# Performance work log

Measured on AMD Instinct MI355X. Metric: run time of the kernel, lower is better.

The kernel has to match this reference:

```python
import jax, jax.numpy as jnp
import numpy as np

D_MODEL = 1024
D_FF = 4 * D_MODEL
NUM_EXPERTS = 8
TOP_K = 2
TOKENS = 4096


def setup_inputs() -> dict:
    key = jax.random.key(0)
    ks = jax.random.split(key, 8)
    s = 0.02
    x = jax.random.normal(ks[0], (TOKENS, D_MODEL), dtype=jnp.float32)
    Wg = jax.random.normal(ks[1], (D_MODEL, NUM_EXPERTS), dtype=jnp.float32) * s
    bg = jnp.zeros((NUM_EXPERTS,), dtype=jnp.float32)
    W1 = jax.random.normal(ks[2], (NUM_EXPERTS, D_MODEL, D_FF), dtype=jnp.float32) * s
    b1 = jnp.zeros((NUM_EXPERTS, D_FF), dtype=jnp.float32)
    W2 = jax.random.normal(ks[3], (NUM_EXPERTS, D_FF, D_MODEL), dtype=jnp.float32) * s
    b2 = jnp.zeros((NUM_EXPERTS, D_MODEL), dtype=jnp.float32)
    return {"x": x, "Wg": Wg, "bg": bg, "W1": W1, "b1": b1, "W2": W2, "b2": b2}


def reference(x, Wg, bg, W1, b1, W2, b2):
    # Gating: softmax over experts, select top-k indices per token.
    gate_scores = jax.nn.softmax(x @ Wg + bg, axis=-1)        # [T, E]
    _, top_k_idx = jax.lax.top_k(gate_scores, TOP_K)          # [T, K]
    # Binary combine mask: 1 where expert selected (top_k indices are distinct).
    # NOTE: original sums selected expert outputs WITHOUT gate weighting.
    mask = jnp.sum(jax.nn.one_hot(top_k_idx, NUM_EXPERTS, dtype=x.dtype), axis=1)  # [T, E]
    out = jnp.zeros_like(x)
    for e in range(NUM_EXPERTS):  # small fixed expert count
        h = jax.nn.relu(x @ W1[e] + b1[e])                    # [T, 4D]
        y = h @ W2[e] + b2[e]                                 # [T, D]
        out = out + mask[:, e:e + 1] * y
    return out
```

## Files before the change

kernel.cpp:

```cpp
#include <hip/hip_runtime.h>
#include <hip/hip_bf16.h>

#define T_TOKENS 4096
#define DM 1024
#define DF 4096
#define NE 8
#define MAXROWS 9216

typedef float f32x4 __attribute__((ext_vector_type(4)));
typedef short bf16x8 __attribute__((ext_vector_type(8)));

__device__ __forceinline__ unsigned short f2bf(float f) {
    union { float f; unsigned int u; } v; v.f = f;
    unsigned int r = v.u + 0x7fffu + ((v.u >> 16) & 1u);
    return (unsigned short)(r >> 16);
}

__device__ __forceinline__ void g2l16(const void* g, void* l) {
    __builtin_amdgcn_global_load_lds(
        (const __attribute__((address_space(1))) void*)g,
        (__attribute__((address_space(3))) void*)l, 16, 0, 0);
}

__global__ __launch_bounds__(256) void gate_kernel(
    const float* __restrict__ x, const float* __restrict__ Wg, const float* __restrict__ bg,
    int* __restrict__ counts, int* __restrict__ topk)
{
    int wave = threadIdx.x >> 6;
    int lane = threadIdx.x & 63;
    int t = blockIdx.x * 4 + wave;
    float acc[NE];
#pragma unroll
    for (int e = 0; e < NE; e++) acc[e] = 0.f;
    const float* xr = x + (size_t)t * DM;
#pragma unroll
    for (int i = 0; i < DM / 64; i++) {
        int d = lane + i * 64;
        float xv = xr[d];
        const float4* wg = (const float4*)(Wg + d * NE);
        float4 w0 = wg[0], w1 = wg[1];
        acc[0] += xv * w0.x; acc[1] += xv * w0.y; acc[2] += xv * w0.z; acc[3] += xv * w0.w;
        acc[4] += xv * w1.x; acc[5] += xv * w1.y; acc[6] += xv * w1.z; acc[7] += xv * w1.w;
    }
#pragma unroll
    for (int e = 0; e < NE; e++) {
#pragma unroll
        for (int off = 32; off > 0; off >>= 1)
            acc[e] += __shfl_down(acc[e], off);
    }
    if (lane == 0) {
        float lg[NE];
#pragma unroll
        for (int e = 0; e < NE; e++) lg[e] = acc[e] + bg[e];
        int b1i = 0; float b1v = lg[0];
        for (int e = 1; e < NE; e++) if (lg[e] > b1v) { b1v = lg[e]; b1i = e; }
        int b2i = -1; float b2v = -1e30f;
        for (int e = 0; e < NE; e++) {
            if (e == b1i) continue;
            if (b2i < 0 || lg[e] > b2v) { b2v = lg[e]; b2i = e; }
        }
        topk[t * 2 + 0] = b1i;
        topk[t * 2 + 1] = b2i;
        atomicAdd(&counts[b1i], 1);
        atomicAdd(&counts[b2i], 1);
    }
}

__global__ __launch_bounds__(256) void scatter_kernel(
    const int* __restrict__ counts, const int* __restrict__ topk,
    int* __restrict__ offsets, int* __restrict__ list)
{
    __shared__ int offs[NE + 1];
    __shared__ int cur[NE];
    if (threadIdx.x == 0) {
        int s = 0;
        for (int e = 0; e < NE; e++) {
            offs[e] = s; offsets[e] = s;
            s += (counts[e] + 127) & ~127;
        }
        offs[NE] = s; offsets[NE] = s;
    }
    if (threadIdx.x < NE) cur[threadIdx.x] = 0;
    __syncthreads();
    for (int i = threadIdx.x; i < T_TOKENS * 2; i += 256) {
        int e = topk[i];
        int pos = atomicAdd(&cur[e], 1);
        list[offs[e] + pos] = i >> 1;
    }
    __syncthreads();
    for (int e = 0; e < NE; e++) {
        int s = offs[e] + counts[e];
        int t = offs[e + 1];
        for (int i = s + threadIdx.x; i < t; i += 256) list[i] = -1;
    }
}

__global__ __launch_bounds__(256) void cvt_x_kernel(
    const float* __restrict__ x, unsigned short* __restrict__ xb)
{
    int i = (blockIdx.x * 256 + threadIdx.x) * 4;
    float4 v = *(const float4*)(x + i);
    unsigned short o[4] = { f2bf(v.x), f2bf(v.y), f2bf(v.z), f2bf(v.w) };
    *(uint2*)(xb + i) = *(const uint2*)o;
}

__global__ __launch_bounds__(256) void tr_cvt_kernel(
    const float* __restrict__ src, unsigned short* __restrict__ dst, int K, int N)
{
    const int e = blockIdx.z;
    src += (size_t)e * K * N;
    dst += (size_t)e * N * K;
    const int n0 = blockIdx.x * 64, k0 = blockIdx.y * 64;
    __shared__ unsigned short tile[64][68];
    const int t = threadIdx.x;
    const int tx = t & 63, ty = t >> 6;
#pragma unroll
    for (int r = 0; r < 16; r++) {
        int k = ty * 16 + r;
        tile[tx][k] = f2bf(src[(size_t)(k0 + k) * N + n0 + tx]);
    }
    __syncthreads();
    const int kx = (t & 15) * 4, ny = t >> 4;
#pragma unroll
    for (int r = 0; r < 4; r++) {
        int n = ny + r * 16;
        *(uint2*)(dst + (size_t)(n0 + n) * K + k0 + kx) = *(const uint2*)&tile[n][kx];
    }
}

__global__ __launch_bounds__(256) void gemm1_kernel(
    const unsigned short* __restrict__ xb, const unsigned short* __restrict__ W1T,
    const float* __restrict__ b1, const int* __restrict__ offsets,
    const int* __restrict__ list, unsigned short* __restrict__ H)
{
    const int total = offsets[NE];
    const int row0 = blockIdx.x * 128;
    if (row0 >= total) return;
    int e = 0;
    while (row0 >= offsets[e + 1]) e++;
    const int n0 = blockIdx.y * 128;

    __shared__ unsigned short Asm[128 * 32];
    __shared__ unsigned short Bsm[128 * 32];

    const int tid = threadIdx.x;
    const int w = tid >> 6, lane = tid & 63;
    const int quad = lane >> 4, l16 = lane & 15;
    const int wm = w >> 1, wn = w & 1;

    const int sr = lane >> 2;
    const int sc = (lane & 3) * 8;
    const int ra1 = 32 * w + sr, ra2 = ra1 + 16;
    int t1 = list[row0 + ra1]; if (t1 < 0) t1 = 0;
    int t2 = list[row0 + ra2]; if (t2 < 0) t2 = 0;
    const unsigned short* gA1 = xb + (size_t)t1 * DM + sc;
    const unsigned short* gA2 = xb + (size_t)t2 * DM + sc;
    const unsigned short* Wb = W1T + (size_t)e * DF * DM;
    const unsigned short* gB1 = Wb + (size_t)(n0 + 32 * w + sr) * DM + sc;
    const unsigned short* gB2 = gB1 + (size_t)16 * DM;
    unsigned short* lA1 = Asm + (2 * w) * 512;
    unsigned short* lA2 = Asm + (2 * w + 1) * 512;
    unsigned short* lB1 = Bsm + (2 * w) * 512;
    unsigned short* lB2 = Bsm + (2 * w + 1) * 512;

    f32x4 acc[4][4];
#pragma unroll
    for (int i = 0; i < 4; i++)
#pragma unroll
        for (int j = 0; j < 4; j++) acc[i][j] = (f32x4){0.f, 0.f, 0.f, 0.f};

    for (int kk = 0; kk < DM; kk += 32) {
        g2l16(gA1 + kk, lA1);
        g2l16(gA2 + kk, lA2);
        g2l16(gB1 + kk, lB1);
        g2l16(gB2 + kk, lB2);
        __syncthreads();
        bf16x8 af[4];
#pragma unroll
        for (int i = 0; i < 4; i++)
            af[i] = *(const bf16x8*)&Asm[(wm * 64 + i * 16 + l16) * 32 + quad * 8];
#pragma unroll
        for (int j = 0; j < 4; j++) {
            bf16x8 bf = *(const bf16x8*)&Bsm[(wn * 64 + j * 16 + l16) * 32 + quad * 8];
#pragma unroll
            for (int i = 0; i < 4; i++)
                acc[i][j] = __builtin_amdgcn_mfma_f32_16x16x32_bf16(af[i], bf, acc[i][j], 0, 0, 0);
        }
        __syncthreads();
    }

    const float* bias = b1 + e * DF;
#pragma unroll
    for (int j = 0; j < 4; j++) {
        int n = n0 + wn * 64 + j * 16 + l16;
        float bj = bias[n];
#pragma unroll
        for (int i = 0; i < 4; i++) {
            int row = row0 + wm * 64 + i * 16 + quad * 4;
#pragma unroll
            for (int r = 0; r < 4; r++) {
                float v = acc[i][j][r] + bj;
                v = fmaxf(v, 0.f);
                H[(size_t)(row + r) * DF + n] = f2bf(v);
            }
        }
    }
}

__global__ __launch_bounds__(256) void gemm2_kernel(
    const unsigned short* __restrict__ H, const unsigned short* __restrict__ W2T,
    const float* __restrict__ b2, const int* __restrict__ offsets,
    const int* __restrict__ list, float* __restrict__ out)
{
    const int total = offsets[NE];
    const int row0 = blockIdx.x * 128;
    if (row0 >= total) return;
    int e = 0;
    while (row0 >= offsets[e + 1]) e++;
    const int n0 = blockIdx.y * 128;

    __shared__ unsigned short Asm[128 * 32];
    __shared__ unsigned short Bsm[128 * 32];

    const int tid = threadIdx.x;
    const int w = tid >> 6, lane = tid & 63;
    const int quad = lane >> 4, l16 = lane & 15;
    const int wm = w >> 1, wn = w & 1;

    const int sr = lane >> 2;
    const int sc = (lane & 3) * 8;
    const unsigned short* gA1 = H + (size_t)(row0 + 32 * w + sr) * DF + sc;
    const unsigned short* gA2 = gA1 + (size_t)16 * DF;
    const unsigned short* Wb = W2T + (size_t)e * DM * DF;
    const unsigned short* gB1 = Wb + (size_t)(n0 + 32 * w + sr) * DF + sc;
    const unsigned short* gB2 = gB1 + (size_t)16 * DF;
    unsigned short* lA1 = Asm + (2 * w) * 512;
    unsigned short* lA2 = Asm + (2 * w + 1) * 512;
    unsigned short* lB1 = Bsm + (2 * w) * 512;
    unsigned short* lB2 = Bsm + (2 * w + 1) * 512;

    f32x4 acc[4][4];
#pragma unroll
    for (int i = 0; i < 4; i++)
#pragma unroll
        for (int j = 0; j < 4; j++) acc[i][j] = (f32x4){0.f, 0.f, 0.f, 0.f};

    for (int kk = 0; kk < DF; kk += 32) {
        g2l16(gA1 + kk, lA1);
        g2l16(gA2 + kk, lA2);
        g2l16(gB1 + kk, lB1);
        g2l16(gB2 + kk, lB2);
        __syncthreads();
        bf16x8 af[4];
#pragma unroll
        for (int i = 0; i < 4; i++)
            af[i] = *(const bf16x8*)&Asm[(wm * 64 + i * 16 + l16) * 32 + quad * 8];
#pragma unroll
        for (int j = 0; j < 4; j++) {
            bf16x8 bf = *(const bf16x8*)&Bsm[(wn * 64 + j * 16 + l16) * 32 + quad * 8];
#pragma unroll
            for (int i = 0; i < 4; i++)
                acc[i][j] = __builtin_amdgcn_mfma_f32_16x16x32_bf16(af[i], bf, acc[i][j], 0, 0, 0);
        }
        __syncthreads();
    }

    const float* bias = b2 + e * DM;
#pragma unroll
    for (int j = 0; j < 4; j++) {
        int n = n0 + wn * 64 + j * 16 + l16;
        float bj = bias[n];
#pragma unroll
        for (int i = 0; i < 4; i++) {
            int row = row0 + wm * 64 + i * 16 + quad * 4;
#pragma unroll
            for (int r = 0; r < 4; r++) {
                int tk = list[row + r];
                if (tk >= 0)
                    atomicAdd(&out[(size_t)tk * DM + n], acc[i][j][r] + bj);
            }
        }
    }
}

extern "C" void kernel_launch(void* const* d_in, const int* in_sizes, int n_in,
                              void* d_out, int out_size, void* d_ws, size_t ws_size,
                              hipStream_t stream)
{
    const float* x  = (const float*)d_in[0];
    const float* Wg = (const float*)d_in[1];
    const float* bg = (const float*)d_in[2];
    const float* W1 = (const float*)d_in[3];
    const float* b1 = (const float*)d_in[4];
    const float* W2 = (const float*)d_in[5];
    const float* b2 = (const float*)d_in[6];
    float* out = (float*)d_out;

    char* ws = (char*)d_ws;
    int* counts  = (int*)(ws + 0);
    int* offsets = (int*)(ws + 64);
    int* topk    = (int*)(ws + 256);
    int* list    = (int*)(ws + 33024);
    unsigned short* xb = (unsigned short*)(ws + (1u << 20));
    unsigned short* WT = (unsigned short*)(ws + (16u << 20));
    unsigned short* Hb = (unsigned short*)(ws + (80u << 20));

    hipMemsetAsync(counts, 0, NE * sizeof(int), stream);
    hipMemsetAsync(d_out, 0, (size_t)out_size * sizeof(float), stream);

    gate_kernel<<<T_TOKENS / 4, 256, 0, stream>>>(x, Wg, bg, counts, topk);
    scatter_kernel<<<1, 256, 0, stream>>>(counts, topk, offsets, list);
    cvt_x_kernel<<<T_TOKENS * DM / 1024, 256, 0, stream>>>(x, xb);

    tr_cvt_kernel<<<dim3(DF / 64, DM / 64, NE), 256, 0, stream>>>(W1, WT, DM, DF);
    gemm1_kernel<<<dim3(MAXROWS / 128, DF / 128), 256, 0, stream>>>(
        xb, WT, b1, offsets, list, Hb);

    tr_cvt_kernel<<<dim3(DM / 64, DF / 64, NE), 256, 0, stream>>>(W2, WT, DF, DM);
    gemm2_kernel<<<dim3(MAXROWS / 128, DM / 128), 256, 0, stream>>>(
        Hb, WT, b2, offsets, list, out);
}
```

Before: 683.5 us.

## Vectorize weight transpose loads, swizzle LDS and block order, shrink gemm2 tile

The weight transpose-convert kernel now reads float4 rows instead of scalar loads, which cuts the number of global load instructions. Both GEMMs XOR-swizzle the 16-byte LDS chunk index to reduce bank conflicts on fragment reads. They also launch on a 1D grid remapped so that blocks scheduled together are spread across the tile space, likely for better XCD/L2 locality. gemm2 uses 64-row tiles instead of 128 to double its block count, since it has only 8 N-tiles, at the cost of more B reloads per row.

```diff
diff --git a/kernel.cpp b/kernel.cpp
--- a/kernel.cpp
+++ b/kernel.cpp
@@ -113,11 +113,16 @@
     const int n0 = blockIdx.x * 64, k0 = blockIdx.y * 64;
     __shared__ unsigned short tile[64][68];
     const int t = threadIdx.x;
-    const int tx = t & 63, ty = t >> 6;
-#pragma unroll
-    for (int r = 0; r < 16; r++) {
-        int k = ty * 16 + r;
-        tile[tx][k] = f2bf(src[(size_t)(k0 + k) * N + n0 + tx]);
+    const int c4 = (t & 15) * 4;
+    const int kr = t >> 4;
+#pragma unroll
+    for (int r = 0; r < 4; r++) {
+        int k = kr + r * 16;
+        float4 v = *(const float4*)(src + (size_t)(k0 + k) * N + n0 + c4);
+        tile[c4 + 0][k] = f2bf(v.x);
+        tile[c4 + 1][k] = f2bf(v.y);
+        tile[c4 + 2][k] = f2bf(v.z);
+        tile[c4 + 3][k] = f2bf(v.w);
     }
     __syncthreads();
     const int kx = (t & 15) * 4, ny = t >> 4;
@@ -133,12 +138,17 @@
     const float* __restrict__ b1, const int* __restrict__ offsets,
     const int* __restrict__ list, unsigned short* __restrict__ H)
 {
+    const int bid = blockIdx.x;
+    const int swz = (bid & 7) * (2304 >> 3) + (bid >> 3);
+    const int bx = swz % (MAXROWS / 128);
+    const int by = swz / (MAXROWS / 128);
+
     const int total = offsets[NE];
-    const int row0 = blockIdx.x * 128;
+    const int row0 = bx * 128;
     if (row0 >= total) return;
     int e = 0;
     while (row0 >= offsets[e + 1]) e++;
-    const int n0 = blockIdx.y * 128;
+    const int n0 = by * 128;
 
     __shared__ unsigned short Asm[128 * 32];
     __shared__ unsigned short Bsm[128 * 32];
@@ -149,7 +159,9 @@
     const int wm = w >> 1, wn = w & 1;
 
     const int sr = lane >> 2;
-    const int sc = (lane & 3) * 8;
+    const int sc = (((lane & 3) ^ ((sr >> 1) & 3))) * 8;
+    const int qx8 = (quad ^ ((l16 >> 1) & 3)) * 8;
+
     const int ra1 = 32 * w + sr, ra2 = ra1 + 16;
     int t1 = list[row0 + ra1]; if (t1 < 0) t1 = 0;
     int t2 = list[row0 + ra2]; if (t2 < 0) t2 = 0;
@@ -178,13 +190,13 @@
         bf16x8 af[4];
 #pragma unroll
         for (int i = 0; i < 4; i++)
-            af[i] = *(const bf16x8*)&Asm[(wm * 64 + i * 16 + l16) * 32 + quad * 8];
+            af[i] = *(const bf16x8*)&Asm[(wm * 64 + i * 16 + l16) * 32 + qx8];
 #pragma unroll
         for (int j = 0; j < 4; j++) {
-            bf16x8 bf = *(const bf16x8*)&Bsm[(wn * 64 + j * 16 + l16) * 32 + quad * 8];
+            bf16x8 bfv = *(const bf16x8*)&Bsm[(wn * 64 + j * 16 + l16) * 32 + qx8];
 #pragma unroll
             for (int i = 0; i < 4; i++)
-                acc[i][j] = __builtin_amdgcn_mfma_f32_16x16x32_bf16(af[i], bf, acc[i][j], 0, 0, 0);
+                acc[i][j] = __builtin_amdgcn_mfma_f32_16x16x32_bf16(af[i], bfv, acc[i][j], 0, 0, 0);
         }
         __syncthreads();
     }
@@ -212,15 +224,20 @@
     const float* __restrict__ b2, const int* __restrict__ offsets,
     const int* __restrict__ list, float* __restrict__ out)
 {
+    const int bid = blockIdx.x;
+    const int swz = (bid & 7) * (1152 >> 3) + (bid >> 3);
+    const int bx = swz % (MAXROWS / 64);
+    const int by = swz / (MAXROWS / 64);
+
     const int total = offsets[NE];
-    const int row0 = blockIdx.x * 128;
+    const int row0 = bx * 64;
     if (row0 >= total) return;
     int e = 0;
     while (row0 >= offsets[e + 1]) e++;
-    const int n0 = blockIdx.y * 128;
-
-    __shared__ unsigned short Asm[128 * 32];
-    __shared__ unsigned short Bsm[128 * 32];
+    const int n0 = by * 128;
+
+    __shared__ unsigned short sA[64 * 32];
+    __shared__ unsigned short sB[128 * 32];
 
     const int tid = threadIdx.x;
     const int w = tid >> 6, lane = tid & 63;
@@ -228,39 +245,38 @@
     const int wm = w >> 1, wn = w & 1;
 
     const int sr = lane >> 2;
-    const int sc = (lane & 3) * 8;
-    const unsigned short* gA1 = H + (size_t)(row0 + 32 * w + sr) * DF + sc;
-    const unsigned short* gA2 = gA1 + (size_t)16 * DF;
+    const int sc = (((lane & 3) ^ ((sr >> 1) & 3))) * 8;
+    const int qx8 = (quad ^ ((l16 >> 1) & 3)) * 8;
+
+    const unsigned short* gA1 = H + (size_t)(row0 + 16 * w + sr) * DF + sc;
     const unsigned short* Wb = W2T + (size_t)e * DM * DF;
     const unsigned short* gB1 = Wb + (size_t)(n0 + 32 * w + sr) * DF + sc;
     const unsigned short* gB2 = gB1 + (size_t)16 * DF;
-    unsigned short* lA1 = Asm + (2 * w) * 512;
-    unsigned short* lA2 = Asm + (2 * w + 1) * 512;
-    unsigned short* lB1 = Bsm + (2 * w) * 512;
-    unsigned short* lB2 = Bsm + (2 * w + 1) * 512;
-
-    f32x4 acc[4][4];
-#pragma unroll
-    for (int i = 0; i < 4; i++)
+    unsigned short* lA1 = sA + w * 512;
+    unsigned short* lB1 = sB + (2 * w) * 512;
+    unsigned short* lB2 = sB + (2 * w + 1) * 512;
+
+    f32x4 acc[2][4];
+#pragma unroll
+    for (int i = 0; i < 2; i++)
 #pragma unroll
         for (int j = 0; j < 4; j++) acc[i][j] = (f32x4){0.f, 0.f, 0.f, 0.f};
 
     for (int kk = 0; kk < DF; kk += 32) {
         g2l16(gA1 + kk, lA1);
-        g2l16(gA2 + kk, lA2);
         g2l16(gB1 + kk, lB1);
         g2l16(gB2 + kk, lB2);
         __syncthreads();
-        bf16x8 af[4];
-#pragma unroll
-        for (int i = 0; i < 4; i++)
-            af[i] = *(const bf16x8*)&Asm[(wm * 64 + i * 16 + l16) * 32 + quad * 8];
+        bf16x8 af[2];
+#pragma unroll
+        for (int i = 0; i < 2; i++)
+            af[i] = *(const bf16x8*)&sA[(wm * 32 + i * 16 + l16) * 32 + qx8];
 #pragma unroll
         for (int j = 0; j < 4; j++) {
-            bf16x8 bf = *(const bf16x8*)&Bsm[(wn * 64 + j * 16 + l16) * 32 + quad * 8];
-#pragma unroll
-            for (int i = 0; i < 4; i++)
-                acc[i][j] = __builtin_amdgcn_mfma_f32_16x16x32_bf16(af[i], bf, acc[i][j], 0, 0, 0);
+            bf16x8 bfv = *(const bf16x8*)&sB[(wn * 64 + j * 16 + l16) * 32 + qx8];
+#pragma unroll
+            for (int i = 0; i < 2; i++)
+                acc[i][j] = __builtin_amdgcn_mfma_f32_16x16x32_bf16(af[i], bfv, acc[i][j], 0, 0, 0);
         }
         __syncthreads();
     }
@@ -271,8 +287,8 @@
         int n = n0 + wn * 64 + j * 16 + l16;
         float bj = bias[n];
 #pragma unroll
-        for (int i = 0; i < 4; i++) {
-            int row = row0 + wm * 64 + i * 16 + quad * 4;
+        for (int i = 0; i < 2; i++) {
+            int row = row0 + wm * 32 + i * 16 + quad * 4;
 #pragma unroll
             for (int r = 0; r < 4; r++) {
                 int tk = list[row + r];
@@ -313,10 +329,10 @@
     cvt_x_kernel<<<T_TOKENS * DM / 1024, 256, 0, stream>>>(x, xb);
 
     tr_cvt_kernel<<<dim3(DF / 64, DM / 64, NE), 256, 0, stream>>>(W1, WT, DM, DF);
-    gemm1_kernel<<<dim3(MAXROWS / 128, DF / 128), 256, 0, stream>>>(
+    gemm1_kernel<<<dim3((MAXROWS / 128) * (DF / 128)), 256, 0, stream>>>(
         xb, WT, b1, offsets, list, Hb);
 
     tr_cvt_kernel<<<dim3(DM / 64, DF / 64, NE), 256, 0, stream>>>(W2, WT, DF, DM);
-    gemm2_kernel<<<dim3(MAXROWS / 128, DM / 128), 256, 0, stream>>>(
+    gemm2_kernel<<<dim3((MAXROWS / 64) * (DM / 128)), 256, 0, stream>>>(
         Hb, WT, b2, offsets, list, out);
 }
```

Result: slower. 725.9 us (+6.2%).
